# Performance work log

Hardware: AMD Instinct MI355X
Metric: run time of the kernel (lower is better)

Reference implementation:

```python
import jax, jax.numpy as jnp
import numpy as np

NQ = 4          # qubits per patch circuit
GRID = 14       # 14x14 grid of 2x2 patches over a 28x28 image
NP = GRID * GRID  # 196 patches
NF = NP * NQ    # 784 features


def setup_inputs() -> dict:
    key = jax.random.key(0)
    k1, k2, k3 = jax.random.split(key, 3)
    x = jax.random.normal(k1, (4096, 1, 28, 28), dtype=jnp.float32)
    patch_params = jax.random.normal(k2, (NQ,), dtype=jnp.float32)
    classifier_params = jax.random.normal(k3, (NF + 1,), dtype=jnp.float32)
    return {"x": x, "patch_params": patch_params, "classifier_params": classifier_params}


def _apply_ry(state, theta, wire):
    # state: [B,P,2,2,2,2] complex, theta: [B,P] real. RY(theta) on `wire`.
    c = jnp.cos(theta * 0.5).astype(state.dtype)
    s = jnp.sin(theta * 0.5).astype(state.dtype)
    gate = jnp.stack([jnp.stack([c, -s], -1), jnp.stack([s, c], -1)], -2)  # [B,P,2,2]
    ax = 2 + wire
    st = jnp.moveaxis(state, ax, 2)
    st = jnp.einsum('bpij,bpj...->bpi...', gate, st)
    return jnp.moveaxis(st, 2, ax)


def _cnot(state, ctrl, tgt):
    # flip target axis on the control=1 slice
    a, b = 2 + ctrl, 2 + tgt
    s0 = jax.lax.index_in_dim(state, 0, axis=a, keepdims=True)
    s1 = jnp.flip(jax.lax.index_in_dim(state, 1, axis=a, keepdims=True), axis=b)
    return jnp.concatenate([s0, s1], axis=a)


def _apply_rz(state, phi, wire):
    # diagonal phase exp(-i*phi/2), exp(+i*phi/2) on `wire` (shared across batch/patches)
    ph = jnp.stack([jnp.exp(-0.5j * phi), jnp.exp(0.5j * phi)]).astype(state.dtype)
    shape = [1] * state.ndim
    shape[2 + wire] = 2
    return state * ph.reshape(shape)


def _quantum_conv(x, patch_params):
    # Batched exact statevector simulation of the 4-qubit patch circuit
    # (RY data encoding -> CNOT chain -> RZ(params) -> <Z_i>) over all
    # 196 patches at once (replaces the Python loop of qnode calls).
    B = x.shape[0]
    # extract non-overlapping 2x2 patches, row-major within each patch
    patches = x[:, 0].reshape(B, GRID, 2, GRID, 2).transpose(0, 1, 3, 2, 4).reshape(B, NP, NQ)
    state = jnp.zeros((B, NP, 2, 2, 2, 2), dtype=jnp.complex64)
    state = state.at[:, :, 0, 0, 0, 0].set(1.0)  # |0000>
    for w in range(NQ):
        state = _apply_ry(state, patches[:, :, w], w)
    for w in range(NQ - 1):
        state = _cnot(state, w, w + 1)
    for w in range(NQ):
        state = _apply_rz(state, patch_params[w], w)
    probs = state.real ** 2 + state.imag ** 2  # [B,P,2,2,2,2]
    sign = jnp.array([1.0, -1.0], dtype=probs.dtype)
    z = []
    for w in range(NQ):
        shape = [1] * probs.ndim
        shape[2 + w] = 2
        z.append(jnp.sum(probs * sign.reshape(shape), axis=(2, 3, 4, 5)))  # <Z_w> [B,P]
    return jnp.stack(z, -1).reshape(B, NF)  # patch-major, qubit-minor (matches torch.cat order)


def reference(x, patch_params, classifier_params):
    feats = _quantum_conv(x, patch_params)               # [B, 784]
    # classifier circuit: sequential RY(f_i * w_i) on one wire compose into a
    # single RY(sum f_i*w_i); trailing RZ(w[-1]) does not change <Z>, so
    # <Z> = cos(angle).
    angle = feats @ classifier_params[:NF]               # [B]
    return jax.nn.sigmoid(jnp.cos(angle))
```

## Files before the change

kernel.cpp:

```cpp
#include <hip/hip_runtime.h>


#define NPATCH 196
#define IMG    784

__global__ __launch_bounds__(256) void fraud_kernel(
    const float* __restrict__ x,
    const float* __restrict__ cp,
    float* __restrict__ out,
    int B)
{
    const int wave = threadIdx.x >> 6;
    const int lane = threadIdx.x & 63;
    const int waveStride = gridDim.x * 4;

    for (int b = blockIdx.x * 4 + wave; b < B; b += waveStride) {
        const float* xb = x + (size_t)b * IMG;

        float acc = 0.f;
        #pragma unroll
        for (int it = 0; it < 4; ++it) {
            const int p = it * 64 + lane;
            if (p < NPATCH) {
                const int gi = p / 14;
                const int gj = p - gi * 14;
                const int base = gi * 56 + gj * 2;
                const float2 r0 = *(const float2*)(xb + base);
                const float2 r1 = *(const float2*)(xb + base + 28);
                const float4 w  = *(const float4*)(cp + 4 * p);
                const float c0 = __cosf(r0.x);
                const float c1 = __cosf(r0.y);
                const float c2 = __cosf(r1.x);
                const float c3 = __cosf(r1.y);
                acc += c0 * fmaf(c1, fmaf(c2, fmaf(c3, w.w, w.z), w.y), w.x);
            }
        }

        #pragma unroll
        for (int off = 32; off > 0; off >>= 1)
            acc += __shfl_down(acc, off, 64);

        if (lane == 0) {
            const float c = cosf(acc);
            out[b] = 1.f / (1.f + __expf(-c));
        }
    }
}

extern "C" void kernel_launch(void* const* d_in, const int* in_sizes, int n_in,
                              void* d_out, int out_size, void* d_ws, size_t ws_size,
                              hipStream_t stream) {
    const float* x  = (const float*)d_in[0];
    const float* cp = (const float*)d_in[2];
    float* out = (float*)d_out;

    const int B = out_size;
    int blocks = (B + 3) / 4;
    if (blocks > 4096) blocks = 4096;
    if (blocks < 1) blocks = 1;
    fraud_kernel<<<blocks, 256, 0, stream>>>(x, cp, out, B);
}
```

Baseline: 64.90 us.

## Map one image per block with cross-wave shared-memory reduction

Reassigns work so each 256-thread block handles one image, with one thread per patch, instead of one wave looping over four patch groups per image. Partial sums from the four waves are combined through shared memory guarded by two block barriers, and the grid grows to one block per image. This removes the per-lane loop and gives more independent memory requests in flight. In exchange, 60 of 256 threads sit idle and each image now pays for barriers and block scheduling.

```diff
diff --git a/kernel.cpp b/kernel.cpp
--- a/kernel.cpp
+++ b/kernel.cpp
@@ -10,40 +10,41 @@
     float* __restrict__ out,
     int B)
 {
-    const int wave = threadIdx.x >> 6;
-    const int lane = threadIdx.x & 63;
-    const int waveStride = gridDim.x * 4;
+    __shared__ float partial[4];
+    const int t    = threadIdx.x;
+    const int lane = t & 63;
+    const int wave = t >> 6;
 
-    for (int b = blockIdx.x * 4 + wave; b < B; b += waveStride) {
+    for (int b = blockIdx.x; b < B; b += gridDim.x) {
         const float* xb = x + (size_t)b * IMG;
 
         float acc = 0.f;
-        #pragma unroll
-        for (int it = 0; it < 4; ++it) {
-            const int p = it * 64 + lane;
-            if (p < NPATCH) {
-                const int gi = p / 14;
-                const int gj = p - gi * 14;
-                const int base = gi * 56 + gj * 2;
-                const float2 r0 = *(const float2*)(xb + base);
-                const float2 r1 = *(const float2*)(xb + base + 28);
-                const float4 w  = *(const float4*)(cp + 4 * p);
-                const float c0 = __cosf(r0.x);
-                const float c1 = __cosf(r0.y);
-                const float c2 = __cosf(r1.x);
-                const float c3 = __cosf(r1.y);
-                acc += c0 * fmaf(c1, fmaf(c2, fmaf(c3, w.w, w.z), w.y), w.x);
-            }
+        if (t < NPATCH) {
+            const int gi = t / 14;
+            const int gj = t - gi * 14;
+            const int base = gi * 56 + gj * 2;
+            const float2 r0 = *(const float2*)(xb + base);
+            const float2 r1 = *(const float2*)(xb + base + 28);
+            const float4 w  = *(const float4*)(cp + 4 * t);
+            acc = __cosf(r0.x) *
+                  fmaf(__cosf(r0.y),
+                       fmaf(__cosf(r1.x),
+                            fmaf(__cosf(r1.y), w.w, w.z), w.y), w.x);
         }
 
         #pragma unroll
         for (int off = 32; off > 0; off >>= 1)
             acc += __shfl_down(acc, off, 64);
 
-        if (lane == 0) {
-            const float c = cosf(acc);
+        if (lane == 0) partial[wave] = acc;
+        __syncthreads();
+
+        if (t == 0) {
+            const float s = partial[0] + partial[1] + partial[2] + partial[3];
+            const float c = cosf(s);
             out[b] = 1.f / (1.f + __expf(-c));
         }
+        __syncthreads();
     }
 }
 
@@ -55,8 +56,8 @@
     float* out = (float*)d_out;
 
     const int B = out_size;
-    int blocks = (B + 3) / 4;
-    if (blocks > 4096) blocks = 4096;
+    int blocks = B;
+    if (blocks > 8192) blocks = 8192;
     if (blocks < 1) blocks = 1;
     fraud_kernel<<<blocks, 256, 0, stream>>>(x, cp, out, B);
 }
```

Result: no change. 63.76 us (-1.8%).
